# Performance work log

Measured on AMD Instinct MI355X. Metric: run time of the kernel, lower is better.

The kernel has to match this reference:

```python
import jax, jax.numpy as jnp
import numpy as np

jax.config.update("jax_enable_x64", True)

# DenseCRF / permutohedral hyperparameters (the 'saved computation' config)
H, W, C = 320, 320, 21
THETA_ALPHA, THETA_BETA, THETA_GAMMA = 80.0, 13.0, 3.0
W_BILATERAL, W_SPATIAL = 10.0, 3.0
N_ITER = 5


def _build_lattice(feats):
    """Permutohedral lattice init: splat offsets os (N,d+1), barycentric ws (N,d+1),
    and blur neighbor index tables n1,n2 of shape (d+1, Mmax), -1 = missing."""
    N, d = feats.shape
    # --- elevate features onto the H_d hyperplane ---
    scale = (np.sqrt(2.0 / 3.0) * (d + 1)) / np.sqrt((np.arange(d) + 1.0) * (np.arange(d) + 2.0))
    cf = feats * jnp.asarray(scale, feats.dtype)                      # (N, d)
    csum = jnp.cumsum(cf[:, ::-1], axis=1)[:, ::-1]                   # suffix sums
    tail = jnp.concatenate([csum[:, 1:], jnp.zeros((N, 1), cf.dtype)], axis=1)
    el = jnp.concatenate([csum[:, :1], tail - jnp.arange(1, d + 1, dtype=cf.dtype) * cf], axis=1)  # (N,d+1)
    # --- nearest zero-colored lattice point (greedy rounding) ---
    down = 1.0 / (d + 1)
    rd = jnp.round(el * down)
    rem0 = rd * (d + 1)                                               # (N, d+1)
    ssum = jnp.sum(rd, axis=1).astype(jnp.int32)
    diff = el - rem0
    di = diff[:, :, None]
    dj = diff[:, None, :]
    ii = jnp.arange(d + 1)[:, None]
    jj = jnp.arange(d + 1)[None, :]
    rank = jnp.sum((dj > di) | ((dj == di) & (jj < ii)), axis=2).astype(jnp.int32) + ssum[:, None]
    rem0 = jnp.where(rank < 0, rem0 + (d + 1), jnp.where(rank > d, rem0 - (d + 1), rem0))
    rank = jnp.where(rank < 0, rank + (d + 1), jnp.where(rank > d, rank - (d + 1), rank))
    # --- barycentric weights ---
    v = (el - rem0) * down
    rows = jnp.arange(N)[:, None]
    b = jnp.zeros((N, d + 2), cf.dtype)
    b = b.at[rows, d - rank].add(v)
    b = b.at[rows, d + 1 - rank].add(-v)
    b = b.at[:, 0].add(1.0 + b[:, d + 1])
    ws = b[:, : d + 1]                                                # (N, d+1)
    # --- lattice keys (first d coords) for the d+1 simplex vertices ---
    key0 = jnp.round(rem0[:, :d]).astype(jnp.int64)
    r = jnp.arange(d + 1, dtype=jnp.int64)[None, :, None]
    rk = rank[:, None, :d].astype(jnp.int64)
    canon = jnp.where(rk < (d + 1) - r, r, r - (d + 1))
    keys = key0[:, None, :] + canon                                   # (N, d+1, d)
    # --- hash keys to unique 1D codes (mixed-radix, covers +-(d+1) neighbor range) ---
    kmin = jnp.min(keys)
    kmax = jnp.max(keys)
    radix = (kmax - kmin) + 2 * d + 2
    shift = kmin - d
    pw = radix ** jnp.arange(d, dtype=jnp.int64)

    def encode(k):
        return jnp.sum((k - shift) * pw, axis=-1)

    codes = encode(keys).reshape(-1)                                  # (N*(d+1),)
    Mmax = codes.shape[0]
    BIG = jnp.iinfo(jnp.int64).max
    uniq, inv = jnp.unique(codes, return_inverse=True, size=Mmax, fill_value=BIG)
    os_ = inv.reshape(N, d + 1).astype(jnp.int32)
    # decode unique lattice keys
    ukeys = (uniq[:, None] // pw[None, :]) % radix + shift            # (Mmax, d)

    def lookup(q):
        i = jnp.clip(jnp.searchsorted(uniq, q), 0, Mmax - 1)
        return jnp.where(uniq[i] == q, i, -1).astype(jnp.int32)

    n1s, n2s = [], []
    for j in range(d + 1):
        ej = (jnp.arange(d) == j).astype(jnp.int64) * (d + 1)         # zero vector when j == d
        n1s.append(lookup(encode(ukeys - 1 + ej)))
        n2s.append(lookup(encode(ukeys + 1 - ej)))
    return os_, ws, jnp.stack(n1s), jnp.stack(n2s)


def _filter(vals_in, os_, ws, n1, n2):
    """Permutohedral splat -> blur -> slice. vals_in: (N, C)."""
    N, C_ = vals_in.shape
    d1, Mmax = n1.shape
    buf = jnp.zeros((Mmax + 1, C_), vals_in.dtype)                    # row 0 = 'missing'
    buf = buf.at[os_.reshape(-1) + 1].add((ws[:, :, None] * vals_in[:, None, :]).reshape(-1, C_))
    for j in range(d1):                                               # blur along each lattice axis
        nb = 0.5 * (buf[n1[j] + 1] + buf[n2[j] + 1])
        buf = buf.at[1:].add(nb)
    alpha = 1.0 / (1.0 + 2.0 ** (-(d1 - 1)))
    return alpha * jnp.sum(ws[:, :, None] * buf[os_ + 1], axis=1)


def _forward(unary, image):
    Hh, Ww, Cc = unary.shape
    N = Hh * Ww
    yy, xx = jnp.meshgrid(jnp.arange(Hh, dtype=jnp.float32), jnp.arange(Ww, dtype=jnp.float32), indexing="ij")
    pos = jnp.stack([xx.ravel(), yy.ravel()], axis=1)                  # (N, 2)
    img = image.reshape(N, -1)
    lat_b = _build_lattice(jnp.concatenate([pos / THETA_ALPHA, img / THETA_BETA], axis=1))  # d=5
    lat_s = _build_lattice(pos / THETA_GAMMA)                          # d=2
    ones = jnp.ones((N, 1), jnp.float32)
    norm_b = _filter(ones, *lat_b) + 1e-20
    norm_s = _filter(ones, *lat_s) + 1e-20
    U = unary.reshape(N, Cc)
    Q = jax.nn.softmax(-U, axis=-1)
    for _ in range(N_ITER):
        msg = W_BILATERAL * (_filter(Q, *lat_b) / norm_b) + W_SPATIAL * (_filter(Q, *lat_s) / norm_s)
        Q = jax.nn.softmax(-U + msg, axis=-1)
    return Q.reshape(Hh, Ww, Cc)


def setup_inputs() -> dict:
    key = jax.random.key(0)
    k1, k2 = jax.random.split(key)
    unary = jax.random.normal(k1, (H, W, C), dtype=jnp.float32)
    image = jax.random.uniform(k2, (H, W, 3), dtype=jnp.float32) * 255.0
    return {"unary": unary, "image": image}


def reference(unary, image):
    return _forward(unary, image)
```

## Files before the change

kernel.cpp:

```cpp
#include <hip/hip_runtime.h>
#include <hip/hip_fp16.h>
#include <cmath>

constexpr int IMH = 320, IMW = 320, NPIX = IMH * IMW, NC = 21;
constexpr int CP4 = 6;
constexpr int DB = 5, DB1 = 6;
constexpr int DS = 2, DS1 = 3;
constexpr int RB = NPIX * DB1;
constexpr int RS = NPIX * DS1;
constexpr int TBS = 1 << 19;
constexpr int NBUCK = 1 << 16;
constexpr int NW1 = (RB + RS) / 64;
constexpr int GS = 512, GN = GS * GS;
constexpr int C0OFF = 16, C1OFF = 200;



#define EMPTY_KEY 0xFFFFFFFFFFFFFFFFULL

__device__ __forceinline__ unsigned long long mix64(unsigned long long x) {
    x ^= x >> 33; x *= 0xff51afd7ed558ccdULL;
    x ^= x >> 33; x *= 0xc4ceb9fe1a85ec53ULL;
    x ^= x >> 33; return x;
}

__device__ __forceinline__ float4 u2f(uint2 u) {
    __half2 a = *reinterpret_cast<__half2*>(&u.x);
    __half2 b = *reinterpret_cast<__half2*>(&u.y);
    float2 fa = __half22float2(a), fb = __half22float2(b);
    return make_float4(fa.x, fa.y, fb.x, fb.y);
}
__device__ __forceinline__ uint2 f2u(float4 v) {
    __half2 a = __floats2half2_rn(v.x, v.y);
    __half2 b = __floats2half2_rn(v.z, v.w);
    uint2 u;
    u.x = *reinterpret_cast<unsigned*>(&a);
    u.y = *reinterpret_cast<unsigned*>(&b);
    return u;
}

__device__ __forceinline__ unsigned pack_ew(int pix, float w) {
    int w15 = (int)lrintf(fminf(fmaxf(w, 0.f), 1.f) * 32767.f);
    return ((unsigned)w15 << 17) | (unsigned)pix;
}
__device__ __forceinline__ void unpack_ew(unsigned e, int& pix, float& w) {
    pix = (int)(e & 0x1FFFFu);
    w = (float)(e >> 17) * (1.0f / 32767.0f);
}

__device__ __forceinline__ void acc8(float* acc, float w, uint4 q) {
    float4 v = u2f(make_uint2(q.x, q.y));
    acc[0] += w * v.x; acc[1] += w * v.y; acc[2] += w * v.z; acc[3] += w * v.w;
    v = u2f(make_uint2(q.z, q.w));
    acc[4] += w * v.x; acc[5] += w * v.y; acc[6] += w * v.z; acc[7] += w * v.w;
}

__device__ __forceinline__ uint4 blur8(uint4 xs, uint4 xa, uint4 xb) {
    float4 s0 = u2f(make_uint2(xs.x, xs.y)), s1 = u2f(make_uint2(xs.z, xs.w));
    float4 a0 = u2f(make_uint2(xa.x, xa.y)), a1 = u2f(make_uint2(xa.z, xa.w));
    float4 b0 = u2f(make_uint2(xb.x, xb.y)), b1 = u2f(make_uint2(xb.z, xb.w));
    s0.x += 0.5f * (a0.x + b0.x); s0.y += 0.5f * (a0.y + b0.y);
    s0.z += 0.5f * (a0.z + b0.z); s0.w += 0.5f * (a0.w + b0.w);
    s1.x += 0.5f * (a1.x + b1.x); s1.y += 0.5f * (a1.y + b1.y);
    s1.z += 0.5f * (a1.z + b1.z); s1.w += 0.5f * (a1.w + b1.w);
    uint2 lo = f2u(s0), hi = f2u(s1);
    return make_uint4(lo.x, lo.y, hi.x, hi.y);
}

__device__ __forceinline__ uint4 pack8(const float* acc) {
    uint2 lo = f2u(make_float4(acc[0], acc[1], acc[2], acc[3]));
    uint2 hi = f2u(make_float4(acc[4], acc[5], acc[6], acc[7]));
    return make_uint4(lo.x, lo.y, hi.x, hi.y);
}

__device__ __forceinline__ int swz8(int bid, int nb) {
    return (bid & 7) * (nb >> 3) + (bid >> 3);
}

template<int D>
__device__ void perm_embed(const float* f, float* bary, unsigned long long* pk) {
    constexpr int D1 = D + 1;
    float cf[D];
    #pragma unroll
    for (int i = 0; i < D; i++) {
        double s = sqrt(2.0 / 3.0) * (double)D1 / sqrt((double)((i + 1) * (i + 2)));
        cf[i] = f[i] * (float)s;
    }
    float csum[D];
    float acc = 0.f;
    #pragma unroll
    for (int i = D - 1; i >= 0; i--) { acc += cf[i]; csum[i] = acc; }
    float el[D1];
    el[0] = csum[0];
    #pragma unroll
    for (int i = 1; i < D; i++) el[i] = csum[i] - (float)i * cf[i - 1];
    el[D] = -(float)D * cf[D - 1];
    const float down = 1.0f / (float)D1;
    float rem0[D1]; int rank[D1]; int ssum = 0;
    #pragma unroll
    for (int i = 0; i < D1; i++) {
        float rd = rintf(el[i] * down);
        rem0[i] = rd * (float)D1;
        ssum += (int)rd;
    }
    float diff[D1];
    #pragma unroll
    for (int i = 0; i < D1; i++) diff[i] = el[i] - rem0[i];
    #pragma unroll
    for (int i = 0; i < D1; i++) {
        int r = 0;
        #pragma unroll
        for (int j = 0; j < D1; j++)
            r += (diff[j] > diff[i]) || ((diff[j] == diff[i]) && (j < i));
        rank[i] = r + ssum;
    }
    #pragma unroll
    for (int i = 0; i < D1; i++) {
        if (rank[i] < 0)      { rank[i] += D1; rem0[i] += (float)D1; }
        else if (rank[i] > D) { rank[i] -= D1; rem0[i] -= (float)D1; }
    }
    float b[D + 2];
    #pragma unroll
    for (int i = 0; i < D + 2; i++) b[i] = 0.f;
    #pragma unroll
    for (int i = 0; i < D1; i++) b[D - rank[i]]     += (el[i] - rem0[i]) * down;
    #pragma unroll
    for (int i = 0; i < D1; i++) b[D + 1 - rank[i]] -= (el[i] - rem0[i]) * down;
    b[0] += 1.0f + b[D + 1];
    #pragma unroll
    for (int i = 0; i < D1; i++) bary[i] = b[i];
    int key0[D];
    #pragma unroll
    for (int i = 0; i < D; i++) key0[i] = (int)rintf(rem0[i]);
    #pragma unroll
    for (int r = 0; r < D1; r++) {
        unsigned long long p = 0;
        #pragma unroll
        for (int i = 0; i < D; i++) {
            int c = key0[i] + ((rank[i] < D1 - r) ? r : r - D1);
            p |= ((unsigned long long)((unsigned)(c + 2048) & 0xFFFu)) << (12 * i);
        }
        pk[r] = p;
    }
}

__device__ __forceinline__ int key_code(unsigned long long k) {
    int c0 = (int)(k & 0xFFFULL);
    int c1 = (int)((k >> 12) & 0xFFFULL);
    return ((c0 & 0xFF) << 8) | (c1 & 0xFF);
}

__device__ __forceinline__ int hash_insert2(ulonglong2* hkid, int tmask, unsigned long long k) {
    int slot = (int)(mix64(k) & (unsigned long long)tmask);
    while (true) {
        unsigned long long prev = atomicCAS(&hkid[slot].x, EMPTY_KEY, k);
        if (prev == EMPTY_KEY || prev == k) return slot;
        slot = (slot + 1) & tmask;
    }
}
__device__ __forceinline__ int hash_lookup2(const ulonglong2* __restrict__ hkid,
                                            int tmask, unsigned long long k) {
    int slot = (int)(mix64(k) & (unsigned long long)tmask);
    while (true) {
        ulonglong2 e = hkid[slot];
        if (e.x == k) return (int)e.y;
        if (e.x == EMPTY_KEY) return -1;
        slot = (slot + 1) & tmask;
    }
}

__global__ void build_both(const float* __restrict__ image, ulonglong2* hkid,
                           int* os, float* wsv, int* pres) {
    int idx = blockIdx.x * blockDim.x + threadIdx.x;
    if (idx < RB) {
        int i = idx / DB1;
        int r = idx - i * DB1;
        int x = i % IMW, y = i / IMW;
        float f[DB];
        f[0] = (float)x / 80.0f;
        f[1] = (float)y / 80.0f;
        f[2] = image[i * 3 + 0] / 13.0f;
        f[3] = image[i * 3 + 1] / 13.0f;
        f[4] = image[i * 3 + 2] / 13.0f;
        float bary[DB1]; unsigned long long pk[DB1];
        perm_embed<DB>(f, bary, pk);
        float w = 0.f; unsigned long long k = 0;
        #pragma unroll
        for (int r2 = 0; r2 < DB1; r2++)
            if (r2 == r) { w = bary[r2]; k = pk[r2]; }
        wsv[idx] = w;
        os[idx] = hash_insert2(hkid, TBS - 1, k);
    } else if (idx < RB + RS) {
        int t = idx - RB;
        int ip = t / DS1;
        int r = t - ip * DS1;
        int x = ip % IMW, y = ip / IMW;
        float f[DS];
        f[0] = (float)x / 3.0f;
        f[1] = (float)y / 3.0f;
        float bary[DS1]; unsigned long long pk[DS1];
        perm_embed<DS>(f, bary, pk);
        float w = 0.f; unsigned long long k = 0;
        #pragma unroll
        for (int r2 = 0; r2 < DS1; r2++)
            if (r2 == r) { w = bary[r2]; k = pk[r2]; }
        int c0 = (int)(k & 0xFFFULL) - 2048;
        int c1 = (int)((k >> 12) & 0xFFFULL) - 2048;
        int gid = (c0 + C0OFF) * GS + (c1 + C1OFF);
        wsv[idx] = w;
        os[idx] = gid;
        pres[gid] = 1;
    }
}

__global__ void hist_b(const ulonglong2* __restrict__ hkid, int* hist) {
    int s = blockIdx.x * blockDim.x + threadIdx.x;
    if (s >= TBS) return;
    unsigned long long k = hkid[s].x;
    if (k == EMPTY_KEY) return;
    atomicAdd(&hist[key_code(k)], 1);
}

__global__ void scan_wave_partial(const int* __restrict__ count, int* incl, int* wsum, int n) {
    int idx = blockIdx.x * blockDim.x + threadIdx.x;
    int lane = threadIdx.x & 63;
    int v = (idx < n) ? count[idx] : 0;
    int s = v;
    #pragma unroll
    for (int d = 1; d < 64; d <<= 1) {
        int t = __shfl_up(s, d);
        if (lane >= d) s += t;
    }
    if (idx < n) incl[idx] = s;
    if (lane == 63) wsum[idx >> 6] = s;
}

__global__ void scan_partials_excl(int* w, int nw, int* total_out) {
    __shared__ int sh[256];
    __shared__ int run;
    if (threadIdx.x == 0) run = 0;
    __syncthreads();
    for (int basei = 0; basei < nw; basei += 256) {
        int idx = basei + threadIdx.x;
        int v = (idx < nw) ? w[idx] : 0;
        sh[threadIdx.x] = v;
        __syncthreads();
        for (int d = 1; d < 256; d <<= 1) {
            int t = (threadIdx.x >= d) ? sh[threadIdx.x - d] : 0;
            __syncthreads();
            sh[threadIdx.x] += t;
            __syncthreads();
        }
        int total = sh[255];
        if (idx < nw) w[idx] = run + sh[threadIdx.x] - v;
        __syncthreads();
        if (threadIdx.x == 0) run += total;
        __syncthreads();
    }
    if (total_out != nullptr && threadIdx.x == 0) *total_out = run;
}

__global__ void scan_finalize(int* off, const int* __restrict__ count,
                              const int* __restrict__ wsum, int n) {
    int idx = blockIdx.x * blockDim.x + threadIdx.x;
    if (idx < n) off[idx] = off[idx] - count[idx] + wsum[idx >> 6];
}

__global__ void assign_b(ulonglong2* hkid, const int* __restrict__ histOff,
                         int* histFill, unsigned long long* uk_b) {
    int s = blockIdx.x * blockDim.x + threadIdx.x;
    if (s >= TBS) return;
    unsigned long long k = hkid[s].x;
    if (k == EMPTY_KEY) return;
    int code = key_code(k);
    int id = histOff[code] + atomicAdd(&histFill[code], 1);
    hkid[s].y = (unsigned long long)id;
    uk_b[id] = k;
}

__global__ void spatial_neighbors(const int* __restrict__ pres, const int* __restrict__ gid2id,
                                  int* __restrict__ n1s, int* __restrict__ n2s) {
    int gid = blockIdx.x * blockDim.x + threadIdx.x;
    if (gid >= GN) return;
    if (!pres[gid]) return;
    int id = gid2id[gid];
    const int d1[3] = {  2 * GS - 1, -GS + 2, -GS - 1 };
    const int d2[3] = { -2 * GS + 1,  GS - 2,  GS + 1 };
    #pragma unroll
    for (int j = 0; j < 3; j++) {
        int g1 = gid + d1[j], g2 = gid + d2[j];
        n1s[j * RS + id] = pres[g1] ? gid2id[g1] : -1;
        n2s[j * RS + id] = pres[g2] ? gid2id[g2] : -1;
    }
}

__global__ void os_count_both(int* os, const ulonglong2* __restrict__ hkid,
                              const int* __restrict__ gid2id, int* cntr, int* rnk) {
    int i = blockIdx.x * blockDim.x + threadIdx.x;
    int lane = threadIdx.x & 63;
    int idg;
    if (i < RB) {
        int id = (int)hkid[os[i]].y;
        os[i] = id;
        idg = id;
    } else {
        int id = gid2id[os[i]];
        os[i] = id;
        idg = RB + id;
    }
    unsigned long long m = 0;
    #pragma unroll
    for (int l = 0; l < 64; l++) {
        int o = __shfl(idg, l);
        m |= (unsigned long long)(o == idg) << l;
    }
    int rless  = __popcll(m & ((1ULL << lane) - 1ULL));
    int leader = __ffsll(m) - 1;
    int gcnt   = __popcll(m);
    int base = 0;
    if (lane == leader) base = atomicAdd(&cntr[idg], gcnt);
    base = __shfl(base, leader);
    rnk[i] = base + rless;
}

__global__ void build_neighbors_b(const unsigned long long* __restrict__ uk,
                                  const ulonglong2* __restrict__ hkid,
                                  const int* cnt, int* n1, int* n2) {
    int Mb = cnt[0];
    int tot = DB1 * Mb;
    int nb = gridDim.x;
    int swb = swz8(blockIdx.x, nb);
    int stride = nb * blockDim.x;
    for (int t = swb * blockDim.x + threadIdx.x; t < tot; t += stride) {
        int j = t / Mb, m = t - j * Mb;
        unsigned long long k = uk[m];
        unsigned long long p1 = 0, p2 = 0;
        #pragma unroll
        for (int i = 0; i < DB; i++) {
            int c = (int)((k >> (12 * i)) & 0xFFFULL) - 2048;
            int a = c + ((i == j) ? DB : -1);
            int b = c + ((i == j) ? -DB : 1);
            p1 |= ((unsigned long long)((unsigned)(a + 2048) & 0xFFFu)) << (12 * i);
            p2 |= ((unsigned long long)((unsigned)(b + 2048) & 0xFFFu)) << (12 * i);
        }
        n1[j * RB + m] = hash_lookup2(hkid, TBS - 1, p1);
        n2[j * RB + m] = hash_lookup2(hkid, TBS - 1, p2);
    }
}

__global__ void compose_b(const int* __restrict__ n1, const int* __restrict__ n2,
                          const int* cnt, int* __restrict__ comp) {
    int Mb = cnt[0];
    int stride = gridDim.x * blockDim.x;
    for (int m = blockIdx.x * blockDim.x + threadIdx.x; m < Mb; m += stride) {
        int a = n1[RB + m], b = n2[RB + m];
        comp[0 * RB + m] = (a < 0) ? -1 : n1[a];
        comp[1 * RB + m] = (a < 0) ? -1 : n2[a];
        comp[2 * RB + m] = (b < 0) ? -1 : n1[b];
        comp[3 * RB + m] = (b < 0) ? -1 : n2[b];
        int a2 = n1[4 * RB + m], b2 = n2[4 * RB + m];
        comp[4 * RB + m] = (a2 < 0) ? -1 : n1[3 * RB + a2];
        comp[5 * RB + m] = (a2 < 0) ? -1 : n2[3 * RB + a2];
        comp[6 * RB + m] = (b2 < 0) ? -1 : n1[3 * RB + b2];
        comp[7 * RB + m] = (b2 < 0) ? -1 : n2[3 * RB + b2];
    }
}
__global__ void compose_s(const int* __restrict__ n1, const int* __restrict__ n2,
                          const int* cnt, int* __restrict__ comp) {
    int Ms = cnt[1];
    int stride = gridDim.x * blockDim.x;
    for (int m = blockIdx.x * blockDim.x + threadIdx.x; m < Ms; m += stride) {
        int a = n1[RS + m], b = n2[RS + m];
        comp[0 * RS + m] = (a < 0) ? -1 : n1[a];
        comp[1 * RS + m] = (a < 0) ? -1 : n2[a];
        comp[2 * RS + m] = (b < 0) ? -1 : n1[b];
        comp[3 * RS + m] = (b < 0) ? -1 : n2[b];
    }
}

__global__ void fill_both(const int* __restrict__ os, const float* __restrict__ wsv,
                          const int* __restrict__ off, const int* __restrict__ rnk,
                          unsigned* epw) {
    int idx = blockIdx.x * blockDim.x + threadIdx.x;
    if (idx >= RB + RS) return;
    int slot, pix;
    if (idx < RB) { slot = os[idx];        pix = idx / DB1; }
    else          { slot = RB + os[idx];   pix = (idx - RB) / DS1; }
    int pos = off[slot] + rnk[idx];
    epw[pos] = pack_ew(pix, wsv[idx]);
}

__global__ void gather_both_h(const uint4* __restrict__ Qh4, const int* __restrict__ off,
                              const int* __restrict__ cntr, const unsigned* __restrict__ epw,
                              uint4* __restrict__ buf4, const int* cnt) {
    int Mb = cnt[0], Ms = cnt[1];
    int totB = Mb + 1;
    int totR = totB + Ms + 1;
    int tot2 = totR * 2;
    int nb = gridDim.x;
    int swb = swz8(blockIdx.x, nb);
    int stride = nb * blockDim.x;
    for (int idx = swb * blockDim.x + threadIdx.x; idx < tot2; idx += stride) {
        int r = idx >> 1, ph = idx & 1;
        int orow, slot;
        if (r < totB) { orow = r; slot = r - 1; }
        else { int t = r - totB; orow = RB + 1 + t; slot = t ? (RB + t - 1) : -1; }
        float acc[24];
        #pragma unroll
        for (int t = 0; t < 24; t++) acc[t] = 0.f;
        if (slot >= 0) {
            int s = off[slot], e = s + cntr[slot];
            for (int t = s + ph; t < e; t += 2) {
                int pix; float w;
                unpack_ew(epw[t], pix, w);
                const uint4* q = Qh4 + (size_t)pix * 3;
                uint4 q0 = q[0], q1 = q[1], q2 = q[2];
                acc8(acc + 0,  w, q0);
                acc8(acc + 8,  w, q1);
                acc8(acc + 16, w, q2);
            }
        }
        #pragma unroll
        for (int t = 0; t < 24; t++) acc[t] += __shfl_xor(acc[t], 1);
        if (ph == 0) {
            size_t b = (size_t)orow * 3;
            #pragma unroll
            for (int t = 0; t < 3; t++)
                buf4[b + t] = pack8(acc + 8 * t);
        }
    }
}

__global__ void blur_both_h(const uint4* __restrict__ in4, uint4* __restrict__ out4,
                            const int* __restrict__ n1b, const int* __restrict__ n2b,
                            const int* __restrict__ n1s, const int* __restrict__ n2s,
                            const int* cnt) {
    int Mb = cnt[0], Ms = cnt[1];
    int totB = (Mb + 1) * 3;
    int tot = totB + (Ms + 1) * 3;
    int nb = gridDim.x;
    int swb = swz8(blockIdx.x, nb);
    int stride = nb * blockDim.x;
    for (int idx = swb * blockDim.x + threadIdx.x; idx < tot; idx += stride) {
        int r, c, orow, a1, a2;
        bool sink;
        if (idx < totB) {
            r = idx / 3; c = idx - r * 3;
            orow = r; sink = (r == 0);
            int m = r - 1;
            a1 = sink ? 0 : n1b[m] + 1;
            a2 = sink ? 0 : n2b[m] + 1;
        } else {
            int t = idx - totB;
            r = t / 3; c = t - r * 3;
            orow = RB + 1 + r; sink = (r == 0);
            int m = r - 1;
            a1 = sink ? 0 : RB + 2 + n1s[m];
            a2 = sink ? 0 : RB + 2 + n2s[m];
        }
        size_t o = (size_t)orow * 3 + c;
        if (sink) { out4[o] = make_uint4(0u, 0u, 0u, 0u); continue; }
        out4[o] = blur8(in4[o], in4[(size_t)a1 * 3 + c], in4[(size_t)a2 * 3 + c]);
    }
}

__global__ void blur_b_h(const uint4* __restrict__ in4, uint4* __restrict__ out4,
                         const int* __restrict__ n1, const int* __restrict__ n2,
                         const int* cnt) {
    int M = cnt[0];
    int tot = (M + 1) * 3;
    int nb = gridDim.x;
    int swb = swz8(blockIdx.x, nb);
    int stride = nb * blockDim.x;
    for (int idx = swb * blockDim.x + threadIdx.x; idx < tot; idx += stride) {
        int r = idx / 3, c = idx - r * 3;
        size_t o = (size_t)r * 3 + c;
        if (r == 0) { out4[o] = make_uint4(0u, 0u, 0u, 0u); continue; }
        int m = r - 1;
        out4[o] = blur8(in4[o], in4[(size_t)(n1[m] + 1) * 3 + c],
                        in4[(size_t)(n2[m] + 1) * 3 + c]);
    }
}

__global__ void fused_blur_both_h(const uint4* __restrict__ in4, uint4* __restrict__ out4,
                                  const int* __restrict__ n1b, const int* __restrict__ n2b,
                                  const int* __restrict__ compb,
                                  const int* __restrict__ n1s, const int* __restrict__ n2s,
                                  const int* __restrict__ comps, const int* cnt) {
    int Mb = cnt[0], Ms = cnt[1];
    int totB = (Mb + 1) * 3;
    int tot = totB + (Ms + 1) * 3;
    int nb = gridDim.x;
    int swb = swz8(blockIdx.x, nb);
    int stride = nb * blockDim.x;
    for (int idx = swb * blockDim.x + threadIdx.x; idx < tot; idx += stride) {
        int r, c, self = 0, i1 = 0, i2 = 0, ia = 0, ib = 0, ic1 = 0, ic2 = 0, ic3 = 0, ic4 = 0;
        bool sink;
        if (idx < totB) {
            r = idx / 3; c = idx - r * 3;
            sink = (r == 0);
            self = r;
            int m = r - 1;
            if (!sink) {
                i1 = n1b[m] + 1;             i2 = n2b[m] + 1;
                ia = n1b[RB + m] + 1;        ib = n2b[RB + m] + 1;
                ic1 = compb[m] + 1;          ic2 = compb[RB + m] + 1;
                ic3 = compb[2 * RB + m] + 1; ic4 = compb[3 * RB + m] + 1;
            }
        } else {
            int t = idx - totB;
            r = t / 3; c = t - r * 3;
            sink = (r == 0);
            self = RB + 1 + r;
            int m = r - 1;
            if (!sink) {
                i1 = RB + 2 + n1s[m];             i2 = RB + 2 + n2s[m];
                ia = RB + 2 + n1s[RS + m];        ib = RB + 2 + n2s[RS + m];
                ic1 = RB + 2 + comps[m];          ic2 = RB + 2 + comps[RS + m];
                ic3 = RB + 2 + comps[2 * RS + m]; ic4 = RB + 2 + comps[3 * RS + m];
            }
        }
        size_t o = (size_t)self * 3 + c;
        if (sink) { out4[o] = make_uint4(0u, 0u, 0u, 0u); continue; }
        float acc[8];
        #pragma unroll
        for (int t2 = 0; t2 < 8; t2++) acc[t2] = 0.f;
        acc8(acc, 1.0f,  in4[o]);
        acc8(acc, 0.5f,  in4[(size_t)i1 * 3 + c]);
        acc8(acc, 0.5f,  in4[(size_t)i2 * 3 + c]);
        acc8(acc, 0.5f,  in4[(size_t)ia * 3 + c]);
        acc8(acc, 0.5f,  in4[(size_t)ib * 3 + c]);
        acc8(acc, 0.25f, in4[(size_t)ic1 * 3 + c]);
        acc8(acc, 0.25f, in4[(size_t)ic2 * 3 + c]);
        acc8(acc, 0.25f, in4[(size_t)ic3 * 3 + c]);
        acc8(acc, 0.25f, in4[(size_t)ic4 * 3 + c]);
        out4[o] = pack8(acc);
    }
}

__global__ void fused_blur_b_h(const uint4* __restrict__ in4, uint4* __restrict__ out4,
                               const int* __restrict__ n1b, const int* __restrict__ n2b,
                               const int* __restrict__ compb, const int* cnt) {
    int M = cnt[0];
    int tot = (M + 1) * 3;
    int nb = gridDim.x;
    int swb = swz8(blockIdx.x, nb);
    int stride = nb * blockDim.x;
    for (int idx = swb * blockDim.x + threadIdx.x; idx < tot; idx += stride) {
        int r = idx / 3, c = idx - r * 3;
        size_t o = (size_t)r * 3 + c;
        if (r == 0) { out4[o] = make_uint4(0u, 0u, 0u, 0u); continue; }
        int m = r - 1;
        int i1 = n1b[3 * RB + m] + 1,  i2 = n2b[3 * RB + m] + 1;
        int ia = n1b[4 * RB + m] + 1,  ib = n2b[4 * RB + m] + 1;
        int ic1 = compb[4 * RB + m] + 1, ic2 = compb[5 * RB + m] + 1;
        int ic3 = compb[6 * RB + m] + 1, ic4 = compb[7 * RB + m] + 1;
        float acc[8];
        #pragma unroll
        for (int t2 = 0; t2 < 8; t2++) acc[t2] = 0.f;
        acc8(acc, 1.0f,  in4[o]);
        acc8(acc, 0.5f,  in4[(size_t)i1 * 3 + c]);
        acc8(acc, 0.5f,  in4[(size_t)i2 * 3 + c]);
        acc8(acc, 0.5f,  in4[(size_t)ia * 3 + c]);
        acc8(acc, 0.5f,  in4[(size_t)ib * 3 + c]);
        acc8(acc, 0.25f, in4[(size_t)ic1 * 3 + c]);
        acc8(acc, 0.25f, in4[(size_t)ic2 * 3 + c]);
        acc8(acc, 0.25f, in4[(size_t)ic3 * 3 + c]);
        acc8(acc, 0.25f, in4[(size_t)ic4 * 3 + c]);
        out4[o] = pack8(acc);
    }
}

__global__ void gather1_both(const int* __restrict__ off, const int* __restrict__ cntr,
                             const unsigned* __restrict__ epw, float* __restrict__ buf,
                             const int* cnt) {
    int Mb = cnt[0], Ms = cnt[1];
    int totB = Mb + 1;
    int tot = totB + Ms + 1;
    int stride = gridDim.x * blockDim.x;
    for (int r = blockIdx.x * blockDim.x + threadIdx.x; r < tot; r += stride) {
        int o, slot;
        if (r < totB) { o = r;              slot = r ? (r - 1) : -1; }
        else          { int t = r - totB; o = RB + 1 + t; slot = t ? (RB + t - 1) : -1; }
        float acc = 0.f;
        if (slot >= 0) {
            int s = off[slot], e = s + cntr[slot];
            for (int t = s; t < e; t++) acc += (float)(epw[t] >> 17) * (1.0f / 32767.0f);
        }
        buf[o] = acc;
    }
}

__global__ void blur1_both(const float* __restrict__ in, float* __restrict__ out,
                           const int* __restrict__ n1b, const int* __restrict__ n2b,
                           const int* __restrict__ n1s, const int* __restrict__ n2s,
                           const int* cnt) {
    int Mb = cnt[0], Ms = cnt[1];
    int totB = Mb + 1;
    int tot = totB + Ms + 1;
    int stride = gridDim.x * blockDim.x;
    for (int r = blockIdx.x * blockDim.x + threadIdx.x; r < tot; r += stride) {
        if (r < totB) {
            if (r == 0) { out[0] = 0.f; continue; }
            int m = r - 1;
            out[r] = in[r] + 0.5f * (in[n1b[m] + 1] + in[n2b[m] + 1]);
        } else {
            int t = r - totB;
            int o = RB + 1 + t;
            if (t == 0) { out[o] = 0.f; continue; }
            int m = t - 1;
            out[o] = in[o] + 0.5f * (in[RB + 2 + n1s[m]] + in[RB + 2 + n2s[m]]);
        }
    }
}

__global__ void blur1_b(const float* __restrict__ in, float* __restrict__ out,
                        const int* __restrict__ n1, const int* __restrict__ n2,
                        const int* cnt) {
    int M = cnt[0];
    int stride = gridDim.x * blockDim.x;
    for (int row = blockIdx.x * blockDim.x + threadIdx.x; row <= M; row += stride) {
        if (row == 0) { out[0] = 0.f; continue; }
        int m = row - 1;
        out[row] = in[row] + 0.5f * (in[n1[m] + 1] + in[n2[m] + 1]);
    }
}

__global__ void fused1_both(const float* __restrict__ in, float* __restrict__ out,
                            const int* __restrict__ n1b, const int* __restrict__ n2b,
                            const int* __restrict__ compb,
                            const int* __restrict__ n1s, const int* __restrict__ n2s,
                            const int* __restrict__ comps, const int* cnt) {
    int Mb = cnt[0], Ms = cnt[1];
    int totB = Mb + 1;
    int tot = totB + Ms + 1;
    int stride = gridDim.x * blockDim.x;
    for (int r = blockIdx.x * blockDim.x + threadIdx.x; r < tot; r += stride) {
        if (r < totB) {
            if (r == 0) { out[0] = 0.f; continue; }
            int m = r - 1;
            out[r] = in[r]
                + 0.5f * (in[n1b[m] + 1] + in[n2b[m] + 1]
                        + in[n1b[RB + m] + 1] + in[n2b[RB + m] + 1])
                + 0.25f * (in[compb[m] + 1] + in[compb[RB + m] + 1]
                         + in[compb[2 * RB + m] + 1] + in[compb[3 * RB + m] + 1]);
        } else {
            int t = r - totB;
            int o = RB + 1 + t;
            if (t == 0) { out[o] = 0.f; continue; }
            int m = t - 1;
            out[o] = in[o]
                + 0.5f * (in[RB + 2 + n1s[m]] + in[RB + 2 + n2s[m]]
                        + in[RB + 2 + n1s[RS + m]] + in[RB + 2 + n2s[RS + m]])
                + 0.25f * (in[RB + 2 + comps[m]] + in[RB + 2 + comps[RS + m]]
                         + in[RB + 2 + comps[2 * RS + m]] + in[RB + 2 + comps[3 * RS + m]]);
        }
    }
}

__global__ void fused1_b(const float* __restrict__ in, float* __restrict__ out,
                         const int* __restrict__ n1b, const int* __restrict__ n2b,
                         const int* __restrict__ compb, const int* cnt) {
    int M = cnt[0];
    int stride = gridDim.x * blockDim.x;
    for (int r = blockIdx.x * blockDim.x + threadIdx.x; r <= M; r += stride) {
        if (r == 0) { out[0] = 0.f; continue; }
        int m = r - 1;
        out[r] = in[r]
            + 0.5f * (in[n1b[3 * RB + m] + 1] + in[n2b[3 * RB + m] + 1]
                    + in[n1b[4 * RB + m] + 1] + in[n2b[4 * RB + m] + 1])
            + 0.25f * (in[compb[4 * RB + m] + 1] + in[compb[5 * RB + m] + 1]
                     + in[compb[6 * RB + m] + 1] + in[compb[7 * RB + m] + 1]);
    }
}

__global__ void slice_norm_both(const float* __restrict__ bufB, const float* __restrict__ bufS,
                                const int* __restrict__ osw, const float* __restrict__ wsv,
                                float* __restrict__ nbv, float* __restrict__ nsv,
                                float alphaB, float alphaS) {
    int i = blockIdx.x * blockDim.x + threadIdx.x;
    if (i >= NPIX) return;
    float sb = 0.f;
    #pragma unroll
    for (int r = 0; r < DB1; r++)
        sb += wsv[i * DB1 + r] * bufB[osw[i * DB1 + r] + 1];
    float ss = 0.f;
    #pragma unroll
    for (int r = 0; r < DS1; r++)
        ss += wsv[RB + i * DS1 + r] * bufS[RB + 2 + osw[RB + i * DS1 + r]];
    nbv[i] = alphaB * sb + 1e-20f;
    nsv[i] = alphaS * ss + 1e-20f;
}

__global__ void slice_update(const float* __restrict__ U,
                             const uint4* __restrict__ bufB4, const uint4* __restrict__ bufS4,
                             const int* __restrict__ osw, const float* __restrict__ wsv,
                             const float* __restrict__ nbv, const float* __restrict__ nsv,
                             float* __restrict__ Q, uint4* __restrict__ Qh4,
                             float alphaB, float alphaS, int use_msg, int write_q) {
    int swb = swz8(blockIdx.x, (int)gridDim.x);
    int i = swb * blockDim.x + threadIdx.x;
    if (i >= NPIX) return;
    float msg[24];
    #pragma unroll
    for (int t = 0; t < 24; t++) msg[t] = 0.f;
    if (use_msg) {
        float ib = 10.0f * alphaB / nbv[i];
        float is = 3.0f * alphaS / nsv[i];
        #pragma unroll
        for (int r = 0; r < DB1; r++) {
            float w = ib * wsv[i * DB1 + r];
            size_t base = (size_t)(osw[i * DB1 + r] + 1) * 3;
            uint4 q0 = bufB4[base], q1 = bufB4[base + 1], q2 = bufB4[base + 2];
            acc8(msg + 0,  w, q0);
            acc8(msg + 8,  w, q1);
            acc8(msg + 16, w, q2);
        }
        #pragma unroll
        for (int r = 0; r < DS1; r++) {
            float w = is * wsv[RB + i * DS1 + r];
            size_t base = (size_t)(RB + 2 + osw[RB + i * DS1 + r]) * 3;
            uint4 q0 = bufS4[base], q1 = bufS4[base + 1], q2 = bufS4[base + 2];
            acc8(msg + 0,  w, q0);
            acc8(msg + 8,  w, q1);
            acc8(msg + 16, w, q2);
        }
    }
    float mx = -1e30f;
    #pragma unroll
    for (int c = 0; c < NC; c++) {
        msg[c] = -U[i * NC + c] + msg[c];
        mx = fmaxf(mx, msg[c]);
    }
    float s = 0.f;
    #pragma unroll
    for (int c = 0; c < NC; c++) { float e = expf(msg[c] - mx); msg[c] = e; s += e; }
    float inv = 1.0f / s;
    #pragma unroll
    for (int c = 0; c < NC; c++) msg[c] *= inv;
    if (write_q) {
        #pragma unroll
        for (int c = 0; c < NC; c++) Q[i * NC + c] = msg[c];
    }
    msg[21] = 0.f; msg[22] = 0.f; msg[23] = 0.f;
    #pragma unroll
    for (int t = 0; t < 3; t++)
        Qh4[i * 3 + t] = pack8(msg + 8 * t);
}

extern "C" void kernel_launch(void* const* d_in, const int* in_sizes, int n_in,
                              void* d_out, int out_size, void* d_ws, size_t ws_size,
                              hipStream_t stream) {
    const float* U     = (const float*)d_in[0];
    const float* image = (const float*)d_in[1];
    float* Q = (float*)d_out;

    char* base = (char*)d_ws;
    size_t off = 0;
    auto alloc = [&](size_t bytes) -> void* {
        off = (off + 255) & ~(size_t)255;
        void* p = base + off; off += bytes; return p;
    };
    int*   osw  = (int*)  alloc((size_t)(RB + RS) * 4);
    float* wsv  = (float*)alloc((size_t)(RB + RS) * 4);
    int*   rnk  = (int*)  alloc((size_t)(RB + RS) * 4);
    int*   n1_b = (int*)  alloc((size_t)DB1 * RB * 4);
    int*   n2_b = (int*)  alloc((size_t)DB1 * RB * 4);
    int*   n1_s = (int*)  alloc((size_t)DS1 * RS * 4);
    int*   n2_s = (int*)  alloc((size_t)DS1 * RS * 4);
    int*   comp_b = (int*)alloc((size_t)8 * RB * 4);
    int*   comp_s = (int*)alloc((size_t)4 * RS * 4);
    unsigned long long* uk_b = (unsigned long long*)alloc((size_t)RB * 8);
    ulonglong2* hkid = (ulonglong2*)alloc((size_t)TBS * 16);
    int*   gid2id = (int*)alloc((size_t)GN * 4);
    int*   cnt  = (int*)  alloc(256);
    int*   histOff = (int*)alloc((size_t)NBUCK * 4);
    int*   wsums   = (int*)alloc((size_t)64 * 1024 * 4);
    int*   wsI     = (int*)alloc((size_t)16384 * 4);
    int*   ws2     = (int*)alloc((size_t)1024 * 4);
    int*   offv    = (int*)alloc((size_t)(RB + RS) * 4);
    char*  zreg  = (char*)alloc((size_t)(RB + RS) * 4 + (size_t)NBUCK * 8 + (size_t)GN * 4);
    int*   cntr     = (int*)zreg;
    int*   hist     = cntr + (RB + RS);
    int*   histFill = hist + NBUCK;
    int*   pres     = histFill + NBUCK;
    size_t zbytes = (size_t)(RB + RS) * 4 + (size_t)NBUCK * 8 + (size_t)GN * 4;
    unsigned* epw = (unsigned*)alloc((size_t)(RB + RS) * 4);
    float* norm_b = (float*)alloc((size_t)NPIX * 4);
    float* norm_s = (float*)alloc((size_t)NPIX * 4);
    uint2* Qh   = (uint2*)alloc((size_t)NPIX * CP4 * 8);
    uint2* buf0 = (uint2*)alloc((size_t)(RB + RS + 2) * CP4 * 8);
    uint2* buf1 = (uint2*)alloc((size_t)(RB + RS + 2) * CP4 * 8);
    float* nbuf0 = (float*)alloc((size_t)(RB + RS + 2) * 4);
    float* nbuf1 = (float*)alloc((size_t)(RB + RS + 2) * 4);
    if (off > ws_size) return;

    const float ALPHA_B = (float)(1.0 / (1.0 + exp2(-(double)DB)));
    const float ALPHA_S = (float)(1.0 / (1.0 + exp2(-(double)DS)));

    constexpr int PGR = 2048;

    hipMemsetAsync(cnt, 0, 16, stream);
    hipMemsetAsync(hkid, 0xFF, (size_t)TBS * 16, stream);
    hipMemsetAsync(zreg, 0, zbytes, stream);

    build_both<<<(RB + RS) / 256, 256, 0, stream>>>(image, hkid, osw, wsv, pres);
    hist_b<<<TBS / 256, 256, 0, stream>>>(hkid, hist);
    scan_wave_partial<<<NBUCK / 256, 256, 0, stream>>>(hist, histOff, wsums, NBUCK);
    scan_partials_excl<<<1, 256, 0, stream>>>(wsums, NBUCK / 64, cnt + 0);
    scan_finalize<<<NBUCK / 256, 256, 0, stream>>>(histOff, hist, wsums, NBUCK);
    assign_b<<<TBS / 256, 256, 0, stream>>>(hkid, histOff, histFill, uk_b);
    scan_wave_partial<<<GN / 256, 256, 0, stream>>>(pres, gid2id, wsums, GN);
    scan_partials_excl<<<1, 256, 0, stream>>>(wsums, GN / 64, cnt + 1);
    scan_finalize<<<GN / 256, 256, 0, stream>>>(gid2id, pres, wsums, GN);
    spatial_neighbors<<<GN / 256, 256, 0, stream>>>(pres, gid2id, n1_s, n2_s);
    compose_s<<<256, 256, 0, stream>>>(n1_s, n2_s, cnt, comp_s);
    os_count_both<<<(RB + RS) / 256, 256, 0, stream>>>(osw, hkid, gid2id, cntr, rnk);
    build_neighbors_b<<<2048, 256, 0, stream>>>(uk_b, hkid, cnt + 0, n1_b, n2_b);
    compose_b<<<1024, 256, 0, stream>>>(n1_b, n2_b, cnt, comp_b);
    scan_wave_partial<<<(RB + RS) / 256, 256, 0, stream>>>(cntr, offv, wsums, RB + RS);
    scan_wave_partial<<<(NW1 + 255) / 256, 256, 0, stream>>>(wsums, wsI, ws2, NW1);
    scan_partials_excl<<<1, 256, 0, stream>>>(ws2, (NW1 + 63) / 64, nullptr);
    scan_finalize<<<(NW1 + 255) / 256, 256, 0, stream>>>(wsI, wsums, ws2, NW1);
    scan_finalize<<<(RB + RS) / 256, 256, 0, stream>>>(offv, cntr, wsI, RB + RS);
    fill_both<<<(RB + RS + 255) / 256, 256, 0, stream>>>(osw, wsv, offv, rnk, epw);

    {
        gather1_both<<<1024, 256, 0, stream>>>(offv, cntr, epw, nbuf0, cnt);
        fused1_both<<<1024, 256, 0, stream>>>(nbuf0, nbuf1, n1_b, n2_b, comp_b,
                                              n1_s, n2_s, comp_s, cnt);
        blur1_both<<<1024, 256, 0, stream>>>(nbuf1, nbuf0,
            n1_b + (size_t)2 * RB, n2_b + (size_t)2 * RB,
            n1_s + (size_t)2 * RS, n2_s + (size_t)2 * RS, cnt);
        fused1_b<<<1024, 256, 0, stream>>>(nbuf0, nbuf1, n1_b, n2_b, comp_b, cnt);
        blur1_b<<<1024, 256, 0, stream>>>(nbuf1, nbuf0,
            n1_b + (size_t)5 * RB, n2_b + (size_t)5 * RB, cnt);
        slice_norm_both<<<(NPIX + 255) / 256, 256, 0, stream>>>(
            nbuf0, nbuf0, osw, wsv, norm_b, norm_s, ALPHA_B, ALPHA_S);
    }

    slice_update<<<(NPIX + 255) / 256, 256, 0, stream>>>(
        U, (const uint4*)buf0, (const uint4*)buf1, osw, wsv, norm_b, norm_s,
        Q, (uint4*)Qh, ALPHA_B, ALPHA_S, 0, 0);

    for (int it = 0; it < 5; it++) {
        gather_both_h<<<PGR, 256, 0, stream>>>((const uint4*)Qh, offv, cntr, epw,
                                               (uint4*)buf0, cnt);
        fused_blur_both_h<<<PGR, 256, 0, stream>>>((const uint4*)buf0, (uint4*)buf1,
            n1_b, n2_b, comp_b, n1_s, n2_s, comp_s, cnt);
        blur_both_h<<<PGR, 256, 0, stream>>>((const uint4*)buf1, (uint4*)buf0,
            n1_b + (size_t)2 * RB, n2_b + (size_t)2 * RB,
            n1_s + (size_t)2 * RS, n2_s + (size_t)2 * RS, cnt);
        fused_blur_b_h<<<PGR, 256, 0, stream>>>((const uint4*)buf0, (uint4*)buf1,
            n1_b, n2_b, comp_b, cnt);
        blur_b_h<<<PGR, 256, 0, stream>>>((const uint4*)buf1, (uint4*)buf0,
            n1_b + (size_t)5 * RB, n2_b + (size_t)5 * RB, cnt);
        slice_update<<<(NPIX + 255) / 256, 256, 0, stream>>>(
            U, (const uint4*)buf0, (const uint4*)buf0, osw, wsv, norm_b, norm_s,
            Q, (uint4*)Qh, ALPHA_B, ALPHA_S, 1, (it == 4) ? 1 : 0);
    }
}
```

Baseline: 736.0 us.

## Fuse bilateral blur axis pairs to cut blur passes from four to three

```diff
diff --git a/kernel.cpp b/kernel.cpp
--- a/kernel.cpp
+++ b/kernel.cpp
@@ -358,11 +358,16 @@
         comp[1 * RB + m] = (a < 0) ? -1 : n2[a];
         comp[2 * RB + m] = (b < 0) ? -1 : n1[b];
         comp[3 * RB + m] = (b < 0) ? -1 : n2[b];
-        int a2 = n1[4 * RB + m], b2 = n2[4 * RB + m];
-        comp[4 * RB + m] = (a2 < 0) ? -1 : n1[3 * RB + a2];
-        comp[5 * RB + m] = (a2 < 0) ? -1 : n2[3 * RB + a2];
-        comp[6 * RB + m] = (b2 < 0) ? -1 : n1[3 * RB + b2];
-        comp[7 * RB + m] = (b2 < 0) ? -1 : n2[3 * RB + b2];
+        int a2 = n1[3 * RB + m], b2 = n2[3 * RB + m];
+        comp[4 * RB + m] = (a2 < 0) ? -1 : n1[2 * RB + a2];
+        comp[5 * RB + m] = (a2 < 0) ? -1 : n2[2 * RB + a2];
+        comp[6 * RB + m] = (b2 < 0) ? -1 : n1[2 * RB + b2];
+        comp[7 * RB + m] = (b2 < 0) ? -1 : n2[2 * RB + b2];
+        int a3 = n1[5 * RB + m], b3 = n2[5 * RB + m];
+        comp[8 * RB + m]  = (a3 < 0) ? -1 : n1[4 * RB + a3];
+        comp[9 * RB + m]  = (a3 < 0) ? -1 : n2[4 * RB + a3];
+        comp[10 * RB + m] = (b3 < 0) ? -1 : n1[4 * RB + b3];
+        comp[11 * RB + m] = (b3 < 0) ? -1 : n2[4 * RB + b3];
     }
 }
 __global__ void compose_s(const int* __restrict__ n1, const int* __restrict__ n2,
@@ -428,57 +433,6 @@
             for (int t = 0; t < 3; t++)
                 buf4[b + t] = pack8(acc + 8 * t);
         }
-    }
-}
-
-__global__ void blur_both_h(const uint4* __restrict__ in4, uint4* __restrict__ out4,
-                            const int* __restrict__ n1b, const int* __restrict__ n2b,
-                            const int* __restrict__ n1s, const int* __restrict__ n2s,
-                            const int* cnt) {
-    int Mb = cnt[0], Ms = cnt[1];
-    int totB = (Mb + 1) * 3;
-    int tot = totB + (Ms + 1) * 3;
-    int nb = gridDim.x;
-    int swb = swz8(blockIdx.x, nb);
-    int stride = nb * blockDim.x;
-    for (int idx = swb * blockDim.x + threadIdx.x; idx < tot; idx += stride) {
-        int r, c, orow, a1, a2;
-        bool sink;
-        if (idx < totB) {
-            r = idx / 3; c = idx - r * 3;
-            orow = r; sink = (r == 0);
-            int m = r - 1;
-            a1 = sink ? 0 : n1b[m] + 1;
-            a2 = sink ? 0 : n2b[m] + 1;
-        } else {
-            int t = idx - totB;
-            r = t / 3; c = t - r * 3;
-            orow = RB + 1 + r; sink = (r == 0);
-            int m = r - 1;
-            a1 = sink ? 0 : RB + 2 + n1s[m];
-            a2 = sink ? 0 : RB + 2 + n2s[m];
-        }
-        size_t o = (size_t)orow * 3 + c;
-        if (sink) { out4[o] = make_uint4(0u, 0u, 0u, 0u); continue; }
-        out4[o] = blur8(in4[o], in4[(size_t)a1 * 3 + c], in4[(size_t)a2 * 3 + c]);
-    }
-}
-
-__global__ void blur_b_h(const uint4* __restrict__ in4, uint4* __restrict__ out4,
-                         const int* __restrict__ n1, const int* __restrict__ n2,
-                         const int* cnt) {
-    int M = cnt[0];
-    int tot = (M + 1) * 3;
-    int nb = gridDim.x;
-    int swb = swz8(blockIdx.x, nb);
-    int stride = nb * blockDim.x;
-    for (int idx = swb * blockDim.x + threadIdx.x; idx < tot; idx += stride) {
-        int r = idx / 3, c = idx - r * 3;
-        size_t o = (size_t)r * 3 + c;
-        if (r == 0) { out4[o] = make_uint4(0u, 0u, 0u, 0u); continue; }
-        int m = r - 1;
-        out4[o] = blur8(in4[o], in4[(size_t)(n1[m] + 1) * 3 + c],
-                        in4[(size_t)(n2[m] + 1) * 3 + c]);
     }
 }
 
@@ -538,9 +492,57 @@
     }
 }
 
+__global__ void fused_blur_b23_s2_h(const uint4* __restrict__ in4, uint4* __restrict__ out4,
+                                    const int* __restrict__ n1b, const int* __restrict__ n2b,
+                                    const int* __restrict__ compb,
+                                    const int* __restrict__ n1s2, const int* __restrict__ n2s2,
+                                    const int* cnt) {
+    int Mb = cnt[0], Ms = cnt[1];
+    int totB = (Mb + 1) * 3;
+    int tot = totB + (Ms + 1) * 3;
+    int nb = gridDim.x;
+    int swb = swz8(blockIdx.x, nb);
+    int stride = nb * blockDim.x;
+    for (int idx = swb * blockDim.x + threadIdx.x; idx < tot; idx += stride) {
+        if (idx < totB) {
+            int r = idx / 3, c = idx - r * 3;
+            size_t o = (size_t)r * 3 + c;
+            if (r == 0) { out4[o] = make_uint4(0u, 0u, 0u, 0u); continue; }
+            int m = r - 1;
+            int i1 = n1b[2 * RB + m] + 1,  i2 = n2b[2 * RB + m] + 1;
+            int ia = n1b[3 * RB + m] + 1,  ib = n2b[3 * RB + m] + 1;
+            int ic1 = compb[4 * RB + m] + 1, ic2 = compb[5 * RB + m] + 1;
+            int ic3 = compb[6 * RB + m] + 1, ic4 = compb[7 * RB + m] + 1;
+            float acc[8];
+            #pragma unroll
+            for (int t2 = 0; t2 < 8; t2++) acc[t2] = 0.f;
+            acc8(acc, 1.0f,  in4[o]);
+            acc8(acc, 0.5f,  in4[(size_t)i1 * 3 + c]);
+            acc8(acc, 0.5f,  in4[(size_t)i2 * 3 + c]);
+            acc8(acc, 0.5f,  in4[(size_t)ia * 3 + c]);
+            acc8(acc, 0.5f,  in4[(size_t)ib * 3 + c]);
+            acc8(acc, 0.25f, in4[(size_t)ic1 * 3 + c]);
+            acc8(acc, 0.25f, in4[(size_t)ic2 * 3 + c]);
+            acc8(acc, 0.25f, in4[(size_t)ic3 * 3 + c]);
+            acc8(acc, 0.25f, in4[(size_t)ic4 * 3 + c]);
+            out4[o] = pack8(acc);
+        } else {
+            int t = idx - totB;
+            int r = t / 3, c = t - r * 3;
+            size_t o = (size_t)(RB + 1 + r) * 3 + c;
+            if (r == 0) { out4[o] = make_uint4(0u, 0u, 0u, 0u); continue; }
+            int m = r - 1;
+            int a1 = RB + 2 + n1s2[m];
+            int a2 = RB + 2 + n2s2[m];
+            out4[o] = blur8(in4[o], in4[(size_t)a1 * 3 + c], in4[(size_t)a2 * 3 + c]);
+        }
+    }
+}
+
 __global__ void fused_blur_b_h(const uint4* __restrict__ in4, uint4* __restrict__ out4,
-                               const int* __restrict__ n1b, const int* __restrict__ n2b,
-                               const int* __restrict__ compb, const int* cnt) {
+                               const int* __restrict__ n1p, const int* __restrict__ n2p,
+                               const int* __restrict__ n1q, const int* __restrict__ n2q,
+                               const int* __restrict__ comp, const int* cnt) {
     int M = cnt[0];
     int tot = (M + 1) * 3;
     int nb = gridDim.x;
@@ -551,10 +553,10 @@
         size_t o = (size_t)r * 3 + c;
         if (r == 0) { out4[o] = make_uint4(0u, 0u, 0u, 0u); continue; }
         int m = r - 1;
-        int i1 = n1b[3 * RB + m] + 1,  i2 = n2b[3 * RB + m] + 1;
-        int ia = n1b[4 * RB + m] + 1,  ib = n2b[4 * RB + m] + 1;
-        int ic1 = compb[4 * RB + m] + 1, ic2 = compb[5 * RB + m] + 1;
-        int ic3 = compb[6 * RB + m] + 1, ic4 = compb[7 * RB + m] + 1;
+        int i1 = n1p[m] + 1,  i2 = n2p[m] + 1;
+        int ia = n1q[m] + 1,  ib = n2q[m] + 1;
+        int ic1 = comp[m] + 1, ic2 = comp[RB + m] + 1;
+        int ic3 = comp[2 * RB + m] + 1, ic4 = comp[3 * RB + m] + 1;
         float acc[8];
         #pragma unroll
         for (int t2 = 0; t2 < 8; t2++) acc[t2] = 0.f;
@@ -588,41 +590,6 @@
             for (int t = s; t < e; t++) acc += (float)(epw[t] >> 17) * (1.0f / 32767.0f);
         }
         buf[o] = acc;
-    }
-}
-
-__global__ void blur1_both(const float* __restrict__ in, float* __restrict__ out,
-                           const int* __restrict__ n1b, const int* __restrict__ n2b,
-                           const int* __restrict__ n1s, const int* __restrict__ n2s,
-                           const int* cnt) {
-    int Mb = cnt[0], Ms = cnt[1];
-    int totB = Mb + 1;
-    int tot = totB + Ms + 1;
-    int stride = gridDim.x * blockDim.x;
-    for (int r = blockIdx.x * blockDim.x + threadIdx.x; r < tot; r += stride) {
-        if (r < totB) {
-            if (r == 0) { out[0] = 0.f; continue; }
-            int m = r - 1;
-            out[r] = in[r] + 0.5f * (in[n1b[m] + 1] + in[n2b[m] + 1]);
-        } else {
-            int t = r - totB;
-            int o = RB + 1 + t;
-            if (t == 0) { out[o] = 0.f; continue; }
-            int m = t - 1;
-            out[o] = in[o] + 0.5f * (in[RB + 2 + n1s[m]] + in[RB + 2 + n2s[m]]);
-        }
-    }
-}
-
-__global__ void blur1_b(const float* __restrict__ in, float* __restrict__ out,
-                        const int* __restrict__ n1, const int* __restrict__ n2,
-                        const int* cnt) {
-    int M = cnt[0];
-    int stride = gridDim.x * blockDim.x;
-    for (int row = blockIdx.x * blockDim.x + threadIdx.x; row <= M; row += stride) {
-        if (row == 0) { out[0] = 0.f; continue; }
-        int m = row - 1;
-        out[row] = in[row] + 0.5f * (in[n1[m] + 1] + in[n2[m] + 1]);
     }
 }
 
@@ -658,19 +625,48 @@
     }
 }
 
+__global__ void fused1_b23_s2(const float* __restrict__ in, float* __restrict__ out,
+                              const int* __restrict__ n1b, const int* __restrict__ n2b,
+                              const int* __restrict__ compb,
+                              const int* __restrict__ n1s2, const int* __restrict__ n2s2,
+                              const int* cnt) {
+    int Mb = cnt[0], Ms = cnt[1];
+    int totB = Mb + 1;
+    int tot = totB + Ms + 1;
+    int stride = gridDim.x * blockDim.x;
+    for (int r = blockIdx.x * blockDim.x + threadIdx.x; r < tot; r += stride) {
+        if (r < totB) {
+            if (r == 0) { out[0] = 0.f; continue; }
+            int m = r - 1;
+            out[r] = in[r]
+                + 0.5f * (in[n1b[2 * RB + m] + 1] + in[n2b[2 * RB + m] + 1]
+                        + in[n1b[3 * RB + m] + 1] + in[n2b[3 * RB + m] + 1])
+                + 0.25f * (in[compb[4 * RB + m] + 1] + in[compb[5 * RB + m] + 1]
+                         + in[compb[6 * RB + m] + 1] + in[compb[7 * RB + m] + 1]);
+        } else {
+            int t = r - totB;
+            int o = RB + 1 + t;
+            if (t == 0) { out[o] = 0.f; continue; }
+            int m = t - 1;
+            out[o] = in[o] + 0.5f * (in[RB + 2 + n1s2[m]] + in[RB + 2 + n2s2[m]]);
+        }
+    }
+}
+
 __global__ void fused1_b(const float* __restrict__ in, float* __restrict__ out,
-                         const int* __restrict__ n1b, const int* __restrict__ n2b,
-                         const int* __restrict__ compb, const int* cnt) {
+                         const int* __restrict__ n1p, const int* __restrict__ n2p,
+                         const int* __restrict__ n1q, const int* __restrict__ n2q,
+                         const int* __restrict__ comp, const int* cnt) {
     int M = cnt[0];
     int stride = gridDim.x * blockDim.x;
     for (int r = blockIdx.x * blockDim.x + threadIdx.x; r <= M; r += stride) {
         if (r == 0) { out[0] = 0.f; continue; }
         int m = r - 1;
         out[r] = in[r]
-            + 0.5f * (in[n1b[3 * RB + m] + 1] + in[n2b[3 * RB + m] + 1]
-                    + in[n1b[4 * RB + m] + 1] + in[n2b[4 * RB + m] + 1])
-            + 0.25f * (in[compb[4 * RB + m] + 1] + in[compb[5 * RB + m] + 1]
-                     + in[compb[6 * RB + m] + 1] + in[compb[7 * RB + m] + 1]);
+            + 0.5f * (in[n1p[m] + 1] + in[n2p[m] + 1]
+                    + in[n1q[m] + 1] + in[n2q[m] + 1])
+            + 0.25f * (in[comp[m] + 1] + in[comp[RB + m] + 1]
+                     + in[comp[2 * RB + m] + 1] + in[comp[3 * RB + m] + 1]);
     }
 }
 
@@ -768,7 +764,7 @@
     int*   n2_b = (int*)  alloc((size_t)DB1 * RB * 4);
     int*   n1_s = (int*)  alloc((size_t)DS1 * RS * 4);
     int*   n2_s = (int*)  alloc((size_t)DS1 * RS * 4);
-    int*   comp_b = (int*)alloc((size_t)8 * RB * 4);
+    int*   comp_b = (int*)alloc((size_t)12 * RB * 4);
     int*   comp_s = (int*)alloc((size_t)4 * RS * 4);
     unsigned long long* uk_b = (unsigned long long*)alloc((size_t)RB * 8);
     ulonglong2* hkid = (ulonglong2*)alloc((size_t)TBS * 16);
@@ -829,14 +825,14 @@
         gather1_both<<<1024, 256, 0, stream>>>(offv, cntr, epw, nbuf0, cnt);
         fused1_both<<<1024, 256, 0, stream>>>(nbuf0, nbuf1, n1_b, n2_b, comp_b,
                                               n1_s, n2_s, comp_s, cnt);
-        blur1_both<<<1024, 256, 0, stream>>>(nbuf1, nbuf0,
-            n1_b + (size_t)2 * RB, n2_b + (size_t)2 * RB,
-            n1_s + (size_t)2 * RS, n2_s + (size_t)2 * RS, cnt);
-        fused1_b<<<1024, 256, 0, stream>>>(nbuf0, nbuf1, n1_b, n2_b, comp_b, cnt);
-        blur1_b<<<1024, 256, 0, stream>>>(nbuf1, nbuf0,
-            n1_b + (size_t)5 * RB, n2_b + (size_t)5 * RB, cnt);
+        fused1_b23_s2<<<1024, 256, 0, stream>>>(nbuf1, nbuf0, n1_b, n2_b, comp_b,
+                                                n1_s + (size_t)2 * RS, n2_s + (size_t)2 * RS, cnt);
+        fused1_b<<<1024, 256, 0, stream>>>(nbuf0, nbuf1,
+            n1_b + (size_t)4 * RB, n2_b + (size_t)4 * RB,
+            n1_b + (size_t)5 * RB, n2_b + (size_t)5 * RB,
+            comp_b + (size_t)8 * RB, cnt);
         slice_norm_both<<<(NPIX + 255) / 256, 256, 0, stream>>>(
-            nbuf0, nbuf0, osw, wsv, norm_b, norm_s, ALPHA_B, ALPHA_S);
+            nbuf1, nbuf0, osw, wsv, norm_b, norm_s, ALPHA_B, ALPHA_S);
     }
 
     slice_update<<<(NPIX + 255) / 256, 256, 0, stream>>>(
@@ -848,15 +844,15 @@
                                                (uint4*)buf0, cnt);
         fused_blur_both_h<<<PGR, 256, 0, stream>>>((const uint4*)buf0, (uint4*)buf1,
             n1_b, n2_b, comp_b, n1_s, n2_s, comp_s, cnt);
-        blur_both_h<<<PGR, 256, 0, stream>>>((const uint4*)buf1, (uint4*)buf0,
-            n1_b + (size_t)2 * RB, n2_b + (size_t)2 * RB,
+        fused_blur_b23_s2_h<<<PGR, 256, 0, stream>>>((const uint4*)buf1, (uint4*)buf0,
+            n1_b, n2_b, comp_b,
             n1_s + (size_t)2 * RS, n2_s + (size_t)2 * RS, cnt);
         fused_blur_b_h<<<PGR, 256, 0, stream>>>((const uint4*)buf0, (uint4*)buf1,
-            n1_b, n2_b, comp_b, cnt);
-        blur_b_h<<<PGR, 256, 0, stream>>>((const uint4*)buf1, (uint4*)buf0,
-            n1_b + (size_t)5 * RB, n2_b + (size_t)5 * RB, cnt);
+            n1_b + (size_t)4 * RB, n2_b + (size_t)4 * RB,
+            n1_b + (size_t)5 * RB, n2_b + (size_t)5 * RB,
+            comp_b + (size_t)8 * RB, cnt);
         slice_update<<<(NPIX + 255) / 256, 256, 0, stream>>>(
-            U, (const uint4*)buf0, (const uint4*)buf0, osw, wsv, norm_b, norm_s,
+            U, (const uint4*)buf1, (const uint4*)buf0, osw, wsv, norm_b, norm_s,
             Q, (uint4*)Qh, ALPHA_B, ALPHA_S, 1, (it == 4) ? 1 : 0);
     }
 }
```

New measurement: 717.4 us. 2.5% less time.
